# Kernel optimization log

Hardware: AMD Instinct MI355X
Metric: run time of the kernel (lower is better)

The kernel has to match this reference:

```python
import jax, jax.numpy as jnp
import numpy as np

N_NODES = 100000
N_EDGES = 1000000
D_NODE = 64
D_EDGE = 64
D_IN = 2 * D_NODE + D_EDGE  # 192, concat of src n_f, s_f, dst n_f
D_OUT = 64


def setup_inputs() -> dict:
    key = jax.random.key(0)
    k1, k2, k3, k4, k5 = jax.random.split(key, 5)
    node_feat = jax.random.normal(k1, (N_NODES, D_NODE), dtype=jnp.float32)
    edge_feat = jax.random.normal(k2, (N_EDGES, D_EDGE), dtype=jnp.float32)
    src_idx = jax.random.randint(k3, (N_EDGES,), 0, N_NODES, dtype=jnp.int64) if jax.config.jax_enable_x64 else jax.random.randint(k3, (N_EDGES,), 0, N_NODES, dtype=jnp.int32)
    dst_idx = jax.random.randint(k4, (N_EDGES,), 0, N_NODES, dtype=jnp.int32)
    src_idx = src_idx.astype(jnp.int32)
    # Kaiming-ish init for the edge MLP (torch Linear default scale ~ 1/sqrt(fan_in))
    W = jax.random.normal(k5, (D_IN, D_OUT), dtype=jnp.float32) / np.sqrt(D_IN)
    b = jnp.zeros((D_OUT,), dtype=jnp.float32)
    return {"node_feat": node_feat, "edge_feat": edge_feat,
            "src_idx": src_idx, "dst_idx": dst_idx, "W": W, "b": b}


def reference(node_feat, edge_feat, src_idx, dst_idx, W, b):
    # EdgeApplyModule.forward: cat([src n_f, s_f, dst n_f], dim=1) -> mlp -> e_f
    feat = jnp.concatenate(
        [node_feat[src_idx], edge_feat, node_feat[dst_idx]], axis=1)  # [E, 192]
    e_f = jax.nn.relu(feat @ W + b)  # Linear(192->64, bias) + ReLU, dropout=0 (eval)
    return e_f
```

## Files before the change

kernel.cpp:

```cpp
#include <hip/hip_runtime.h>
#include <hip/hip_bf16.h>


typedef __attribute__((ext_vector_type(8))) short short8;
typedef __attribute__((ext_vector_type(4))) float f32x4;

#define D 64
#define DIN 192
#define BM 64
#define GRID 2048

__device__ __forceinline__ short bf_bits(float f) {
  __hip_bfloat16 h = __float2bfloat16(f);
  union { __hip_bfloat16 b; short s; } u; u.b = h;
  return u.s;
}

__global__ void prep_W_kernel(const float* __restrict__ W,
                              unsigned short* __restrict__ wsB) {
  int i = blockIdx.x * blockDim.x + threadIdx.x;
  if (i >= DIN * D) return;
  int k = i >> 6;
  int n = i & 63;
  int t = k >> 5;
  int g = (k >> 3) & 3;
  int s = k & 7;
  int c = n >> 4;
  int l = g * 16 + (n & 15);
  wsB[(((t << 2) + c) * 64 + l) * 8 + s] = (unsigned short)bf_bits(W[i]);
}

__global__ __launch_bounds__(256, 4) void edge_mlp_kernel(
    const float* __restrict__ node_feat,
    const float* __restrict__ edge_feat,
    const int*   __restrict__ src_idx,
    const int*   __restrict__ dst_idx,
    const unsigned short* __restrict__ wsB,
    const float* __restrict__ bias,
    float* __restrict__ out,
    int nE) {
  const int tid = threadIdx.x;
  const int w = tid >> 6;
  const int l = tid & 63;
  const int g = l >> 4;
  const int r = l & 15;
  const int rowIC = w * 16 + r;
  const int gofs = g * 8;

  const short8* B = reinterpret_cast<const short8*>(wsB);
  const int nChunks = (nE + BM - 1) / BM;
  const int G = gridDim.x;

  const float bn0 = bias[r], bn1 = bias[16 + r], bn2 = bias[32 + r],
              bn3 = bias[48 + r];

  float4 X[12];
  int si1, di1, ec1;

  int c = blockIdx.x;

  {
    long e0 = (long)c * BM + rowIC;
    int eL = e0 < nE ? (int)e0 : nE - 1;
    si1 = src_idx[eL];
    di1 = dst_idx[eL];
    ec1 = eL;
  }
  {
    const float* pS = node_feat + (size_t)si1 * D + gofs;
    const float* pE = edge_feat + (size_t)ec1 * D + gofs;
    const float* pD = node_feat + (size_t)di1 * D + gofs;
    X[0]  = *reinterpret_cast<const float4*>(pS);
    X[1]  = *reinterpret_cast<const float4*>(pS + 4);
    X[2]  = *reinterpret_cast<const float4*>(pS + 32);
    X[3]  = *reinterpret_cast<const float4*>(pS + 36);
    X[4]  = *reinterpret_cast<const float4*>(pE);
    X[5]  = *reinterpret_cast<const float4*>(pE + 4);
    X[6]  = *reinterpret_cast<const float4*>(pE + 32);
    X[7]  = *reinterpret_cast<const float4*>(pE + 36);
    X[8]  = *reinterpret_cast<const float4*>(pD);
    X[9]  = *reinterpret_cast<const float4*>(pD + 4);
    X[10] = *reinterpret_cast<const float4*>(pD + 32);
    X[11] = *reinterpret_cast<const float4*>(pD + 36);
  }
  {
    long e1 = (long)(c + G) * BM + rowIC;
    int eL = e1 < nE ? (int)e1 : nE - 1;
    si1 = src_idx[eL];
    di1 = dst_idx[eL];
    ec1 = eL;
  }

  for (; c < nChunks; c += G) {
    short8 A[6];
    #pragma unroll
    for (int t = 0; t < 6; ++t) {
      float4 x = X[2 * t], y = X[2 * t + 1];
      A[t][0] = bf_bits(x.x); A[t][1] = bf_bits(x.y);
      A[t][2] = bf_bits(x.z); A[t][3] = bf_bits(x.w);
      A[t][4] = bf_bits(y.x); A[t][5] = bf_bits(y.y);
      A[t][6] = bf_bits(y.z); A[t][7] = bf_bits(y.w);
    }

    if (c + G < nChunks) {
      const float* pS = node_feat + (size_t)si1 * D + gofs;
      const float* pE = edge_feat + (size_t)ec1 * D + gofs;
      const float* pD = node_feat + (size_t)di1 * D + gofs;
      X[0]  = *reinterpret_cast<const float4*>(pS);
      X[1]  = *reinterpret_cast<const float4*>(pS + 4);
      X[2]  = *reinterpret_cast<const float4*>(pS + 32);
      X[3]  = *reinterpret_cast<const float4*>(pS + 36);
      X[4]  = *reinterpret_cast<const float4*>(pE);
      X[5]  = *reinterpret_cast<const float4*>(pE + 4);
      X[6]  = *reinterpret_cast<const float4*>(pE + 32);
      X[7]  = *reinterpret_cast<const float4*>(pE + 36);
      X[8]  = *reinterpret_cast<const float4*>(pD);
      X[9]  = *reinterpret_cast<const float4*>(pD + 4);
      X[10] = *reinterpret_cast<const float4*>(pD + 32);
      X[11] = *reinterpret_cast<const float4*>(pD + 36);

      long e2 = (long)(c + 2 * G) * BM + rowIC;
      int eL = e2 < nE ? (int)e2 : nE - 1;
      si1 = src_idx[eL];
      di1 = dst_idx[eL];
      ec1 = eL;
    }

    int bofs = 0;
    asm volatile("" : "+v"(bofs));
    const short8* B2 = B + bofs;

    f32x4 acc[4];
    #pragma unroll
    for (int cc = 0; cc < 4; ++cc) acc[cc] = (f32x4){0.f, 0.f, 0.f, 0.f};

    #pragma unroll
    for (int t = 0; t < 6; ++t) {
      short8 b0 = B2[(t * 4 + 0) * 64 + l];
      short8 b1 = B2[(t * 4 + 1) * 64 + l];
      short8 b2 = B2[(t * 4 + 2) * 64 + l];
      short8 b3 = B2[(t * 4 + 3) * 64 + l];
      acc[0] = __builtin_amdgcn_mfma_f32_16x16x32_bf16(A[t], b0, acc[0], 0, 0, 0);
      acc[1] = __builtin_amdgcn_mfma_f32_16x16x32_bf16(A[t], b1, acc[1], 0, 0, 0);
      acc[2] = __builtin_amdgcn_mfma_f32_16x16x32_bf16(A[t], b2, acc[2], 0, 0, 0);
      acc[3] = __builtin_amdgcn_mfma_f32_16x16x32_bf16(A[t], b3, acc[3], 0, 0, 0);
    }

    const long baseW = (long)c * BM + w * 16;
    const float bns[4] = {bn0, bn1, bn2, bn3};
    #pragma unroll
    for (int cc = 0; cc < 4; ++cc) {
      const int n = cc * 16 + r;
      #pragma unroll
      for (int j = 0; j < 4; ++j) {
        long eo = baseW + g * 4 + j;
        if (eo < nE) {
          float v = acc[cc][j] + bns[cc];
          out[eo * D + n] = v > 0.f ? v : 0.f;
        }
      }
    }
  }
}

extern "C" void kernel_launch(void* const* d_in, const int* in_sizes, int n_in,
                              void* d_out, int out_size, void* d_ws, size_t ws_size,
                              hipStream_t stream) {
  const float* node_feat = (const float*)d_in[0];
  const float* edge_feat = (const float*)d_in[1];
  const int*   src_idx   = (const int*)d_in[2];
  const int*   dst_idx   = (const int*)d_in[3];
  const float* W         = (const float*)d_in[4];
  const float* bias      = (const float*)d_in[5];
  float* out = (float*)d_out;
  unsigned short* wsB = (unsigned short*)d_ws;

  const int nE = in_sizes[2];

  hipLaunchKernelGGL(prep_W_kernel, dim3((DIN * D + 255) / 256), dim3(256), 0,
                     stream, W, wsB);

  const int nChunks = (nE + BM - 1) / BM;
  const int grid = nChunks < GRID ? nChunks : GRID;
  hipLaunchKernelGGL(edge_mlp_kernel, dim3(grid), dim3(256), 0, stream,
                     node_feat, edge_feat, src_idx, dst_idx, wsB, bias, out, nE);
}
```

Before: 541.9 us.

## Stage gathered features via global_load_lds and keep bf16 W in shared memory

Gathered node and edge feature rows now go directly into per-wave LDS buffers through global_load_lds instead of register prefetch. The pre-swizzled bf16 weight matrix is loaded once per block into LDS rather than read from global memory each chunk. Grid size and launch-bounds occupancy are lowered to fit the larger LDS footprint. This cuts register pressure and repeated weight loads, but adds full vmcnt/lgkmcnt waits and lowers occupancy, which may reduce latency hiding for this bandwidth-bound gather.

```diff
diff --git a/kernel.cpp b/kernel.cpp
--- a/kernel.cpp
+++ b/kernel.cpp
@@ -8,12 +8,18 @@
 #define D 64
 #define DIN 192
 #define BM 64
-#define GRID 2048
+#define GRID 512
 
 __device__ __forceinline__ short bf_bits(float f) {
   __hip_bfloat16 h = __float2bfloat16(f);
   union { __hip_bfloat16 b; short s; } u; u.b = h;
   return u.s;
+}
+
+__device__ __forceinline__ void gll16(const void* g, void* l) {
+  __builtin_amdgcn_global_load_lds(
+      (const __attribute__((address_space(1))) void*)g,
+      (__attribute__((address_space(3))) void*)l, 16, 0, 0);
 }
 
 __global__ void prep_W_kernel(const float* __restrict__ W,
@@ -30,7 +36,7 @@
   wsB[(((t << 2) + c) * 64 + l) * 8 + s] = (unsigned short)bf_bits(W[i]);
 }
 
-__global__ __launch_bounds__(256, 4) void edge_mlp_kernel(
+__global__ __launch_bounds__(256, 2) void edge_mlp_kernel(
     const float* __restrict__ node_feat,
     const float* __restrict__ edge_feat,
     const int*   __restrict__ src_idx,
@@ -39,6 +45,9 @@
     const float* __restrict__ bias,
     float* __restrict__ out,
     int nE) {
+  __shared__ short8 Bs[24][64];
+  __shared__ float  Xs[4][12][64][4];
+
   const int tid = threadIdx.x;
   const int w = tid >> 6;
   const int l = tid & 63;
@@ -47,88 +56,92 @@
   const int rowIC = w * 16 + r;
   const int gofs = g * 8;
 
-  const short8* B = reinterpret_cast<const short8*>(wsB);
+  {
+    const short8* Bsrc = reinterpret_cast<const short8*>(wsB);
+    short8* Bdst = &Bs[0][0];
+    for (int j = tid; j < 24 * 64; j += 256) Bdst[j] = Bsrc[j];
+  }
+  __syncthreads();
+
   const int nChunks = (nE + BM - 1) / BM;
   const int G = gridDim.x;
 
   const float bn0 = bias[r], bn1 = bias[16 + r], bn2 = bias[32 + r],
               bn3 = bias[48 + r];
 
-  float4 X[12];
-  int si1, di1, ec1;
-
   int c = blockIdx.x;
 
+  int siN, diN, ecN;
   {
     long e0 = (long)c * BM + rowIC;
     int eL = e0 < nE ? (int)e0 : nE - 1;
-    si1 = src_idx[eL];
-    di1 = dst_idx[eL];
-    ec1 = eL;
-  }
-  {
-    const float* pS = node_feat + (size_t)si1 * D + gofs;
-    const float* pE = edge_feat + (size_t)ec1 * D + gofs;
-    const float* pD = node_feat + (size_t)di1 * D + gofs;
-    X[0]  = *reinterpret_cast<const float4*>(pS);
-    X[1]  = *reinterpret_cast<const float4*>(pS + 4);
-    X[2]  = *reinterpret_cast<const float4*>(pS + 32);
-    X[3]  = *reinterpret_cast<const float4*>(pS + 36);
-    X[4]  = *reinterpret_cast<const float4*>(pE);
-    X[5]  = *reinterpret_cast<const float4*>(pE + 4);
-    X[6]  = *reinterpret_cast<const float4*>(pE + 32);
-    X[7]  = *reinterpret_cast<const float4*>(pE + 36);
-    X[8]  = *reinterpret_cast<const float4*>(pD);
-    X[9]  = *reinterpret_cast<const float4*>(pD + 4);
-    X[10] = *reinterpret_cast<const float4*>(pD + 32);
-    X[11] = *reinterpret_cast<const float4*>(pD + 36);
+    int si = src_idx[eL];
+    int di = dst_idx[eL];
+    const float* pS = node_feat + (size_t)si * D + gofs;
+    const float* pE = edge_feat + (size_t)eL * D + gofs;
+    const float* pD = node_feat + (size_t)di * D + gofs;
+    gll16(pS,      &Xs[w][0][0][0]);
+    gll16(pS + 4,  &Xs[w][1][0][0]);
+    gll16(pS + 32, &Xs[w][2][0][0]);
+    gll16(pS + 36, &Xs[w][3][0][0]);
+    gll16(pE,      &Xs[w][4][0][0]);
+    gll16(pE + 4,  &Xs[w][5][0][0]);
+    gll16(pE + 32, &Xs[w][6][0][0]);
+    gll16(pE + 36, &Xs[w][7][0][0]);
+    gll16(pD,      &Xs[w][8][0][0]);
+    gll16(pD + 4,  &Xs[w][9][0][0]);
+    gll16(pD + 32, &Xs[w][10][0][0]);
+    gll16(pD + 36, &Xs[w][11][0][0]);
   }
   {
     long e1 = (long)(c + G) * BM + rowIC;
     int eL = e1 < nE ? (int)e1 : nE - 1;
-    si1 = src_idx[eL];
-    di1 = dst_idx[eL];
-    ec1 = eL;
+    siN = src_idx[eL];
+    diN = dst_idx[eL];
+    ecN = eL;
   }
 
   for (; c < nChunks; c += G) {
+    asm volatile("s_waitcnt vmcnt(0)" ::: "memory");
+    __builtin_amdgcn_sched_barrier(0);
+
     short8 A[6];
     #pragma unroll
     for (int t = 0; t < 6; ++t) {
-      float4 x = X[2 * t], y = X[2 * t + 1];
+      float4 x = *reinterpret_cast<const float4*>(&Xs[w][2 * t][l][0]);
+      float4 y = *reinterpret_cast<const float4*>(&Xs[w][2 * t + 1][l][0]);
       A[t][0] = bf_bits(x.x); A[t][1] = bf_bits(x.y);
       A[t][2] = bf_bits(x.z); A[t][3] = bf_bits(x.w);
       A[t][4] = bf_bits(y.x); A[t][5] = bf_bits(y.y);
       A[t][6] = bf_bits(y.z); A[t][7] = bf_bits(y.w);
     }
 
+    asm volatile("s_waitcnt lgkmcnt(0)" ::: "memory");
+    __builtin_amdgcn_sched_barrier(0);
+
     if (c + G < nChunks) {
-      const float* pS = node_feat + (size_t)si1 * D + gofs;
-      const float* pE = edge_feat + (size_t)ec1 * D + gofs;
-      const float* pD = node_feat + (size_t)di1 * D + gofs;
-      X[0]  = *reinterpret_cast<const float4*>(pS);
-      X[1]  = *reinterpret_cast<const float4*>(pS + 4);
-      X[2]  = *reinterpret_cast<const float4*>(pS + 32);
-      X[3]  = *reinterpret_cast<const float4*>(pS + 36);
-      X[4]  = *reinterpret_cast<const float4*>(pE);
-      X[5]  = *reinterpret_cast<const float4*>(pE + 4);
-      X[6]  = *reinterpret_cast<const float4*>(pE + 32);
-      X[7]  = *reinterpret_cast<const float4*>(pE + 36);
-      X[8]  = *reinterpret_cast<const float4*>(pD);
-      X[9]  = *reinterpret_cast<const float4*>(pD + 4);
-      X[10] = *reinterpret_cast<const float4*>(pD + 32);
-      X[11] = *reinterpret_cast<const float4*>(pD + 36);
+      const float* pS = node_feat + (size_t)siN * D + gofs;
+      const float* pE = edge_feat + (size_t)ecN * D + gofs;
+      const float* pD = node_feat + (size_t)diN * D + gofs;
+      gll16(pS,      &Xs[w][0][0][0]);
+      gll16(pS + 4,  &Xs[w][1][0][0]);
+      gll16(pS + 32, &Xs[w][2][0][0]);
+      gll16(pS + 36, &Xs[w][3][0][0]);
+      gll16(pE,      &Xs[w][4][0][0]);
+      gll16(pE + 4,  &Xs[w][5][0][0]);
+      gll16(pE + 32, &Xs[w][6][0][0]);
+      gll16(pE + 36, &Xs[w][7][0][0]);
+      gll16(pD,      &Xs[w][8][0][0]);
+      gll16(pD + 4,  &Xs[w][9][0][0]);
+      gll16(pD + 32, &Xs[w][10][0][0]);
+      gll16(pD + 36, &Xs[w][11][0][0]);
 
       long e2 = (long)(c + 2 * G) * BM + rowIC;
       int eL = e2 < nE ? (int)e2 : nE - 1;
-      si1 = src_idx[eL];
-      di1 = dst_idx[eL];
-      ec1 = eL;
-    }
-
-    int bofs = 0;
-    asm volatile("" : "+v"(bofs));
-    const short8* B2 = B + bofs;
+      siN = src_idx[eL];
+      diN = dst_idx[eL];
+      ecN = eL;
+    }
 
     f32x4 acc[4];
     #pragma unroll
@@ -136,10 +149,10 @@
 
     #pragma unroll
     for (int t = 0; t < 6; ++t) {
-      short8 b0 = B2[(t * 4 + 0) * 64 + l];
-      short8 b1 = B2[(t * 4 + 1) * 64 + l];
-      short8 b2 = B2[(t * 4 + 2) * 64 + l];
-      short8 b3 = B2[(t * 4 + 3) * 64 + l];
+      short8 b0 = Bs[t * 4 + 0][l];
+      short8 b1 = Bs[t * 4 + 1][l];
+      short8 b2 = Bs[t * 4 + 2][l];
+      short8 b3 = Bs[t * 4 + 3][l];
       acc[0] = __builtin_amdgcn_mfma_f32_16x16x32_bf16(A[t], b0, acc[0], 0, 0, 0);
       acc[1] = __builtin_amdgcn_mfma_f32_16x16x32_bf16(A[t], b1, acc[1], 0, 0, 0);
       acc[2] = __builtin_amdgcn_mfma_f32_16x16x32_bf16(A[t], b2, acc[2], 0, 0, 0);
```

Result: faster. 482.8 us (-10.9%).
